# Kernel tuning notes

Hardware: AMD Instinct MI355X
Metric: run time of the kernel (lower is better)

The kernel has to match this reference:

```python
import jax, jax.numpy as jnp
import numpy as np

B, T, H, F, E = 512, 32, 768, 3072, 3  # E = num_route_experts = num_experts - 1 (top-1 beam)


def setup_inputs() -> dict:
    key = jax.random.key(0)
    ks = jax.random.split(key, 4)
    s = 0.02
    return {
        "x": jax.random.normal(ks[0], (B, T, H), jnp.float32),
        "Wg": jax.random.normal(ks[1], (E, H), jnp.float32) * s,
        "W1": jax.random.normal(ks[2], (E, H, F), jnp.float32) * s,
        "b1": jnp.zeros((E, F), jnp.float32),
        "W2": jax.random.normal(ks[3], (E, F, H), jnp.float32) * s,
        "b2": jnp.zeros((E, H), jnp.float32),
    }


def reference(x, Wg, W1, b1, W2, b2):
    # forward_gate: mean-pool over tokens (attention_mask is all-ones), linear gate, softmax
    scores = jax.nn.softmax(jnp.mean(x, axis=1) @ Wg.T, axis=-1)  # [B, E]
    # beam_search, first layer with num_route_beam=1: plain top-1 expert selection
    _, idx = jax.lax.top_k(scores, 1)
    sel = idx[:, 0]  # [B] int32, selected expert per sample
    # forward_expert_ffn: densely run EVERY route expert (gelu MLP) on the full batch
    h = jax.nn.gelu(jnp.einsum('bth,ehf->betf', x, W1) + b1[None, :, None, :], approximate=False)  # [B,E,T,F]
    y = jnp.einsum('betf,efh->beth', h, W2) + b2[None, :, None, :]  # [B,E,T,H]
    # weight_type == 'ffn_prob': one-hot mask times gate prob, then sum over experts
    w = scores * jax.nn.one_hot(sel, E, dtype=scores.dtype)  # [B, E]
    out = jnp.einsum('beth,be->bth', y, w)  # [B, T, H]
    return out
```

## Files before the change

kernel.cpp:

```cpp
#include <hip/hip_runtime.h>
#include <hip/hip_bf16.h>
#include <cstdint>
#include <cstddef>

namespace {

constexpr int kB = 512, kT = 32, kH = 768, kF = 3072, kE = 3;
constexpr int kMaxTiles = 131;
constexpr int kMaxChunk = 131;
constexpr int kXPermTile = 128 * kH;
constexpr int kHbufTile  = 128 * kF;

typedef __attribute__((ext_vector_type(8))) short short8;
typedef __attribute__((ext_vector_type(4))) float f32x4;

__device__ __forceinline__ void gld_lds16(const void* g, void* l) {
  __builtin_amdgcn_global_load_lds(
      (const __attribute__((address_space(1))) void*)g,
      (__attribute__((address_space(3))) void*)l, 16, 0, 0);
}

__device__ __forceinline__ float bf2f(__hip_bfloat16 v) { return __bfloat162float(v); }
__device__ __forceinline__ float bfu(unsigned short u) {
  return __uint_as_float(((unsigned)u) << 16);
}
__device__ __forceinline__ unsigned short f2bfb(float f) {
  __hip_bfloat16 h = __float2bfloat16(f);
  return *reinterpret_cast<unsigned short*>(&h);
}

__device__ __forceinline__ float gelu_f(float v) {
  float av = fabsf(v);
  float z = av * 0.70710678118654752f;
  float t = __builtin_amdgcn_rcpf(fmaf(0.3275911f, z, 1.0f));
  float p = fmaf(fmaf(fmaf(fmaf(1.061405429f, t, -1.453152027f), t, 1.421413741f),
                      t, -0.284496736f), t, 0.254829592f) * t;
  float er = fmaf(-p, __expf(-z * z), 1.0f);
  return 0.5f * v + 0.5f * av * er;
}

__global__ void k_sniff_all(const unsigned short* __restrict__ x,
                            const unsigned short* __restrict__ g,
                            const unsigned short* __restrict__ w1,
                            const unsigned short* __restrict__ w2,
                            int* __restrict__ flags, int* __restrict__ cnt,
                            int* __restrict__ ticket) {
  int bb = blockIdx.x;
  if (bb == 0 && threadIdx.x < 4) {
    if (threadIdx.x < 3) cnt[threadIdx.x] = 0;
    else *ticket = 0;
  }
  const unsigned short* p = (bb == 0) ? x : (bb == 1) ? g : (bb == 2) ? w1 : w2;
  int nwords = (bb == 1) ? kE * kH : 4096;
  __shared__ int cnt_s;
  if (threadIdx.x == 0) cnt_s = 0;
  __syncthreads();
  int local = 0;
  for (int i = threadIdx.x; i < nwords; i += 256) {
    unsigned e = (p[i] >> 7) & 0xFF;
    if (e >= 0xC0) ++local;
  }
  atomicAdd(&cnt_s, local);
  __syncthreads();
  if (threadIdx.x == 0) flags[bb] = (cnt_s > 64) ? 1 : 0;
}

__global__ void k_route(const void* __restrict__ xv, const void* __restrict__ Wgv,
                        const int* __restrict__ flags,
                        float* __restrict__ wsel,
                        int* __restrict__ cnt, int* __restrict__ lists,
                        int* __restrict__ ticket,
                        int* __restrict__ tileExpert, int* __restrict__ tileBatch,
                        int* __restrict__ numTiles) {
  bool fx = (flags[0] != 0), fg = (flags[1] != 0);
  int b = blockIdx.x;
  int tid = threadIdx.x;
  float a0 = 0.f, a1 = 0.f, a2 = 0.f;
  if (tid < 192) {
    float m0 = 0.f, m1 = 0.f, m2 = 0.f, m3 = 0.f;
    if (fx) {
      const float4* xr = (const float4*)((const float*)xv + (size_t)b * kT * kH) + tid;
#pragma unroll 8
      for (int t = 0; t < kT; ++t) {
        float4 u = xr[t * 192];
        m0 += u.x; m1 += u.y; m2 += u.z; m3 += u.w;
      }
    } else {
      const ushort4* xr = (const ushort4*)((const unsigned short*)xv + (size_t)b * kT * kH) + tid;
#pragma unroll 8
      for (int t = 0; t < kT; ++t) {
        ushort4 u = xr[t * 192];
        m0 += bfu(u.x); m1 += bfu(u.y); m2 += bfu(u.z); m3 += bfu(u.w);
      }
    }
    const float inv = 1.f / kT;
    m0 *= inv; m1 *= inv; m2 *= inv; m3 *= inv;
#pragma unroll
    for (int e = 0; e < kE; ++e) {
      float w0, w1v, w2v, w3;
      int base = e * kH + tid * 4;
      if (fg) {
        float4 u = *(const float4*)((const float*)Wgv + base);
        w0 = u.x; w1v = u.y; w2v = u.z; w3 = u.w;
      } else {
        ushort4 u = *(const ushort4*)((const unsigned short*)Wgv + base);
        w0 = bfu(u.x); w1v = bfu(u.y); w2v = bfu(u.z); w3 = bfu(u.w);
      }
      float d = m0 * w0 + m1 * w1v + m2 * w2v + m3 * w3;
      if (e == 0) a0 = d; else if (e == 1) a1 = d; else a2 = d;
    }
  }
  __shared__ float red[3][256];
  red[0][tid] = a0; red[1][tid] = a1; red[2][tid] = a2;
  __syncthreads();
  for (int s2 = 128; s2 > 0; s2 >>= 1) {
    if (tid < s2) {
      red[0][tid] += red[0][tid + s2];
      red[1][tid] += red[1][tid + s2];
      red[2][tid] += red[2][tid + s2];
    }
    __syncthreads();
  }
  if (tid == 0) {
    float l0 = red[0][0], l1 = red[1][0], l2 = red[2][0];
    int am = 0; float mx = l0;
    if (l1 > mx) { mx = l1; am = 1; }
    if (l2 > mx) { mx = l2; am = 2; }
    float e0 = expf(l0 - mx), e1 = expf(l1 - mx), e2 = expf(l2 - mx);
    float inv = 1.f / (e0 + e1 + e2);
    float sc = (am == 0 ? e0 : (am == 1 ? e1 : e2)) * inv;
    wsel[b] = sc;
    int pos = atomicAdd(&cnt[am], 1);
    lists[am * kB + pos] = b;
    __threadfence();
    int tk = atomicAdd(ticket, 1);
    if (tk == kB - 1) {
      __threadfence();
      int t = 0;
      for (int e = 0; e < kE; ++e) {
        int c = cnt[e];
        for (int i = 0; i < c; i += 4) {
          tileExpert[t] = e;
          for (int s = 0; s < 4; ++s)
            tileBatch[t * 4 + s] = (i + s < c) ? lists[e * kB + i + s] : -1;
          ++t;
        }
      }
      *numTiles = t;
      for (int tt = t; tt < kMaxTiles; ++tt) {
        tileExpert[tt] = 0;
        for (int s = 0; s < 4; ++s) tileBatch[tt * 4 + s] = -1;
      }
    }
  }
}

__global__ __launch_bounds__(256)
void k_transpose6(const void* __restrict__ w1src, const void* __restrict__ w2src,
                  __hip_bfloat16* __restrict__ w1dst, __hip_bfloat16* __restrict__ w2dst,
                  const int* __restrict__ flags) {
  int z = blockIdx.z;
  bool isW1 = (z < 3);
  int e = isW1 ? z : z - 3;
  bool f32 = (flags[isW1 ? 2 : 3] != 0);
  const float* sf = (const float*)(isW1 ? w1src : w2src);
  const unsigned short* sb = (const unsigned short*)(isW1 ? w1src : w2src);
  unsigned short* dst = (unsigned short*)(isW1 ? w1dst : w2dst);
  int K = isW1 ? kH : kF, N = isW1 ? kF : kH;
  int ntx = N / 64;
  int bx = blockIdx.x;
  int n0 = (bx % ntx) * 64, k0 = (bx / ntx) * 64;
  __shared__ __align__(16) unsigned short t[64][73];
  size_t eoff = (size_t)e * K * N;
  int tr = threadIdx.x >> 4;
  int tc4 = (threadIdx.x & 15) * 4;
#pragma unroll
  for (int i = 0; i < 4; ++i) {
    int r = tr + 16 * i;
    size_t idx = eoff + (size_t)(k0 + r) * N + n0 + tc4;
    if (f32) {
      float4 u = *(const float4*)(sf + idx);
      t[r][tc4] = f2bfb(u.x); t[r][tc4 + 1] = f2bfb(u.y);
      t[r][tc4 + 2] = f2bfb(u.z); t[r][tc4 + 3] = f2bfb(u.w);
    } else {
      ushort4 u = *(const ushort4*)(sb + idx);
      t[r][tc4] = u.x; t[r][tc4 + 1] = u.y; t[r][tc4 + 2] = u.z; t[r][tc4 + 3] = u.w;
    }
  }
  __syncthreads();
#pragma unroll
  for (int i = 0; i < 4; ++i) {
    int rn = tr + 16 * i;
    ushort4 v;
    v.x = t[tc4][rn]; v.y = t[tc4 + 1][rn]; v.z = t[tc4 + 2][rn]; v.w = t[tc4 + 3][rn];
    *(ushort4*)(dst + eoff + (size_t)(n0 + rn) * K + k0 + tc4) = v;
  }
}

__global__ __launch_bounds__(256)
void k_convert_x(const void* __restrict__ xv, const int* __restrict__ flags,
                 const int* __restrict__ tileBatch, const int* __restrict__ numTiles,
                 __hip_bfloat16* __restrict__ xperm) {
  int tile = blockIdx.y;
  if (tile >= *numTiles) return;
  int kblk = blockIdx.x;
  bool fx = (flags[0] != 0);
  const float* xf = (const float*)xv;
  const __hip_bfloat16* xb = (const __hip_bfloat16*)xv;
  int tb0 = tileBatch[tile * 4];
  int tb[4];
#pragma unroll
  for (int s = 0; s < 4; ++s) {
    int bb = tileBatch[tile * 4 + s];
    tb[s] = (bb < 0) ? tb0 : bb;
  }
  int tid = threadIdx.x;
  short8* dst = (short8*)(xperm + (size_t)tile * kXPermTile + kblk * 8192);
#pragma unroll
  for (int i = 0; i < 4; ++i) {
    int s = i * 256 + tid;
    int m = (s >> 2) & 127, kk = s >> 9;
    int q = (s & 3) ^ ((s >> 3) & 3);
    int row = tb[m >> 5] * kT + (m & 31);
    size_t src = (size_t)row * kH + kblk * 64 + kk * 32 + q * 8;
    short8 v;
    if (fx) {
      float4 u = *(const float4*)(xf + src);
      float4 w = *(const float4*)(xf + src + 4);
      v[0] = f2bfb(u.x); v[1] = f2bfb(u.y); v[2] = f2bfb(u.z); v[3] = f2bfb(u.w);
      v[4] = f2bfb(w.x); v[5] = f2bfb(w.y); v[6] = f2bfb(w.z); v[7] = f2bfb(w.w);
    } else {
      v = *(const short8*)(xb + src);
    }
    dst[s] = v;
  }
}

__global__ __launch_bounds__(256, 2)
void k_ffn1(const __hip_bfloat16* __restrict__ xperm,
            const __hip_bfloat16* __restrict__ w1t,
            const __hip_bfloat16* __restrict__ b1,
            const int* __restrict__ tileExpert,
            const int* __restrict__ numTiles,
            int tileOff,
            __hip_bfloat16* __restrict__ hbuf) {
  int j = blockIdx.y;
  int local = j / 3;
  int tile = local + tileOff;
  if (tile >= *numTiles) return;
  int nIdx = 8 * (j % 3) + blockIdx.x;
  int nbase = nIdx * 128;
  int e = tileExpert[tile];
  __shared__ __align__(16) short ldsbuf[16384];
  short* ldsA = ldsbuf;
  short* ldsB = ldsbuf + 8192;
  int tid = threadIdx.x;
  int lane = tid & 63, wid = tid >> 6;
  int wm = wid >> 1, wn = wid & 1;
  int lane16 = lane & 15, qf = lane >> 4;
  int swzl = (lane16 >> 1) & 3;
  int qx = (qf ^ swzl) * 8;

  f32x4 acc[4][4];
#pragma unroll
  for (int r = 0; r < 4; ++r)
#pragma unroll
    for (int c = 0; c < 4; ++c) acc[r][c] = (f32x4)0.f;

  const __hip_bfloat16* w1e = w1t + (size_t)e * kF * kH;
  const __hip_bfloat16* xtile = xperm + (size_t)tile * kXPermTile;
  const __hip_bfloat16* gB[4];
  short* lA[4];
  short* lB[4];
  int aoff[4];
#pragma unroll
  for (int it = 0; it < 4; ++it) {
    int s = it * 256 + tid;
    int m = (s >> 2) & 127, kk = s >> 9;
    int q = (s & 3) ^ ((s >> 3) & 3);
    aoff[it] = s * 8;
    gB[it] = w1e + (size_t)(nbase + m) * kH + kk * 32 + q * 8;
    lA[it] = &ldsA[s * 8];
    lB[it] = &ldsB[s * 8];
  }

  for (int k0 = 0; k0 < kH; k0 += 64) {
#pragma unroll
    for (int it = 0; it < 4; ++it) gld_lds16(xtile + k0 * 128 + aoff[it], lA[it]);
#pragma unroll
    for (int it = 0; it < 4; ++it) gld_lds16(gB[it] + k0, lB[it]);
    __syncthreads();
#pragma unroll
    for (int kk = 0; kk < 2; ++kk) {
      short8 af[4], bfr[4];
#pragma unroll
      for (int r = 0; r < 4; ++r) {
        int mr = wm * 64 + r * 16 + lane16;
        af[r] = *(const short8*)&ldsA[(kk * 512 + mr * 4) * 8 + qx];
      }
#pragma unroll
      for (int c = 0; c < 4; ++c) {
        int mb = wn * 64 + c * 16 + lane16;
        bfr[c] = *(const short8*)&ldsB[(kk * 512 + mb * 4) * 8 + qx];
      }
#pragma unroll
      for (int r = 0; r < 4; ++r)
#pragma unroll
        for (int c = 0; c < 4; ++c)
          acc[r][c] = __builtin_amdgcn_mfma_f32_16x16x32_bf16(af[r], bfr[c], acc[r][c], 0, 0, 0);
    }
    __syncthreads();
  }

  __hip_bfloat16* htile = hbuf + (size_t)local * kHbufTile;
  unsigned short* uls = (unsigned short*)ldsbuf;
  int q4 = qf * 4;
#pragma unroll
  for (int c = 0; c < 4; ++c) {
    int nn = wn * 64 + c * 16 + lane16;
    float bias = bf2f(b1[e * kF + nbase + nn]);
    int lbase = (nn >> 6) * 8192 + ((nn >> 5) & 1) * 4096 + (nn & 7);
    int qn = (nn >> 3) & 3;
#pragma unroll
    for (int r = 0; r < 4; ++r) {
#pragma unroll
      for (int g = 0; g < 4; ++g) {
        int m = wm * 64 + r * 16 + q4 + g;
        float v = acc[r][c][g] + bias;
        uls[lbase + (m * 4 + (qn ^ ((m >> 1) & 3))) * 8] = f2bfb(gelu_f(v));
      }
    }
  }
  __syncthreads();
  unsigned short* dstg = (unsigned short*)htile + (size_t)(nbase >> 6) * 8192;
#pragma unroll
  for (int i = 0; i < 8; ++i) {
    int s = i * 2048 + tid * 8;
    *(short8*)(dstg + s) = *(const short8*)(uls + s);
  }
}

__global__ __launch_bounds__(256, 2)
void k_ffn2(const __hip_bfloat16* __restrict__ hbuf,
            const __hip_bfloat16* __restrict__ w2t,
            const __hip_bfloat16* __restrict__ b2,
            const float* __restrict__ wsel,
            const int* __restrict__ tileExpert,
            const int* __restrict__ tileBatch,
            const int* __restrict__ numTiles,
            int tileOff, int chunk,
            float* __restrict__ out) {
  int j = blockIdx.y;
  int local = blockIdx.x + 8 * (j / 6);
  if (local >= chunk) return;
  int tile = local + tileOff;
  if (tile >= *numTiles) return;
  int nbase = (j % 6) * 128;
  int e = tileExpert[tile];
  int tbraw[4];
  float sc[4];
#pragma unroll
  for (int s = 0; s < 4; ++s) {
    int bb = tileBatch[tile * 4 + s];
    tbraw[s] = bb;
    sc[s] = (bb >= 0) ? wsel[bb] : 0.f;
  }
  __shared__ __align__(16) short ldsA[8192];
  __shared__ __align__(16) short ldsB[8192];
  int tid = threadIdx.x;
  int lane = tid & 63, wid = tid >> 6;
  int wm = wid >> 1, wn = wid & 1;
  int lane16 = lane & 15, qf = lane >> 4;
  int swzl = (lane16 >> 1) & 3;
  int qx = (qf ^ swzl) * 8;

  f32x4 acc[4][4];
#pragma unroll
  for (int r = 0; r < 4; ++r)
#pragma unroll
    for (int c = 0; c < 4; ++c) acc[r][c] = (f32x4)0.f;

  const __hip_bfloat16* w2e = w2t + (size_t)e * kF * kH;
  const __hip_bfloat16* htile = hbuf + (size_t)local * kHbufTile;
  const __hip_bfloat16* gB[4];
  short* lA[4];
  short* lB[4];
  int aoff[4];
#pragma unroll
  for (int it = 0; it < 4; ++it) {
    int s = it * 256 + tid;
    int m = (s >> 2) & 127, kk = s >> 9;
    int q = (s & 3) ^ ((s >> 3) & 3);
    aoff[it] = s * 8;
    gB[it] = w2e + (size_t)(nbase + m) * kF + kk * 32 + q * 8;
    lA[it] = &ldsA[s * 8];
    lB[it] = &ldsB[s * 8];
  }

  for (int k0 = 0; k0 < kF; k0 += 64) {
#pragma unroll
    for (int it = 0; it < 4; ++it) gld_lds16(htile + k0 * 128 + aoff[it], lA[it]);
#pragma unroll
    for (int it = 0; it < 4; ++it) gld_lds16(gB[it] + k0, lB[it]);
    __syncthreads();
#pragma unroll
    for (int kk = 0; kk < 2; ++kk) {
      short8 af[4], bfr[4];
#pragma unroll
      for (int r = 0; r < 4; ++r) {
        int mr = wm * 64 + r * 16 + lane16;
        af[r] = *(const short8*)&ldsA[(kk * 512 + mr * 4) * 8 + qx];
      }
#pragma unroll
      for (int c = 0; c < 4; ++c) {
        int mb = wn * 64 + c * 16 + lane16;
        bfr[c] = *(const short8*)&ldsB[(kk * 512 + mb * 4) * 8 + qx];
      }
#pragma unroll
      for (int r = 0; r < 4; ++r)
#pragma unroll
        for (int c = 0; c < 4; ++c)
          acc[r][c] = __builtin_amdgcn_mfma_f32_16x16x32_bf16(af[r], bfr[c], acc[r][c], 0, 0, 0);
    }
    __syncthreads();
  }

  int q4 = qf * 4;
#pragma unroll
  for (int c = 0; c < 4; ++c) {
    int ncol = wn * 64 + c * 16 + lane16;
    float bias = bf2f(b2[e * kH + nbase + ncol]);
#pragma unroll
    for (int r = 0; r < 4; ++r) {
      int s = (wm * 64 + r * 16) >> 5;
      int bb = tbraw[s];
      if (bb < 0) continue;
      float scale = sc[s];
#pragma unroll
      for (int g = 0; g < 4; ++g) {
        int m = wm * 64 + r * 16 + q4 + g;
        float v = (acc[r][c][g] + bias) * scale;
        out[((size_t)(bb * kT + (m & 31))) * kH + nbase + ncol] = v;
      }
    }
  }
}

}

extern "C" void kernel_launch(void* const* d_in, const int* in_sizes, int n_in,
                              void* d_out, int out_size, void* d_ws, size_t ws_size,
                              hipStream_t stream) {
  (void)in_sizes; (void)n_in; (void)out_size;
  float* out = (float*)d_out;

  char* ws = (char*)d_ws;
  size_t off = 0;
  auto alloc = [&](size_t bytes) -> char* {
    char* p = ws + off;
    off = (off + bytes + 255) & ~(size_t)255;
    return p;
  };
  int*   flags      = (int*)alloc(16);
  int*   cnt        = (int*)alloc(kE * 4);
  int*   ticket     = (int*)alloc(4);
  float* wsel       = (float*)alloc(kB * 4);
  int*   lists      = (int*)alloc((size_t)kE * kB * 4);
  int*   tileExpert = (int*)alloc(kMaxTiles * 4);
  int*   tileBatch  = (int*)alloc(kMaxTiles * 4 * 4);
  int*   numTiles   = (int*)alloc(4);
  __hip_bfloat16* w1t   = (__hip_bfloat16*)alloc((size_t)kE * kH * kF * 2);
  __hip_bfloat16* w2t   = (__hip_bfloat16*)alloc((size_t)kE * kH * kF * 2);
  __hip_bfloat16* xperm = (__hip_bfloat16*)alloc((size_t)kMaxTiles * kXPermTile * 2);

  size_t tileBytes = (size_t)kHbufTile * 2;
  size_t avail = (ws_size > off + tileBytes) ? (ws_size - off) : tileBytes;
  int chunk = (int)(avail / tileBytes);
  if (chunk > kMaxChunk) chunk = kMaxChunk;
  if (chunk < 1) chunk = 1;
  __hip_bfloat16* hbuf = (__hip_bfloat16*)alloc((size_t)chunk * tileBytes);

  k_sniff_all<<<4, 256, 0, stream>>>((const unsigned short*)d_in[0],
                                     (const unsigned short*)d_in[1],
                                     (const unsigned short*)d_in[2],
                                     (const unsigned short*)d_in[4],
                                     flags, cnt, ticket);
  k_route<<<kB, 256, 0, stream>>>(d_in[0], d_in[1], flags, wsel, cnt, lists,
                                  ticket, tileExpert, tileBatch, numTiles);
  k_transpose6<<<dim3(576, 1, 6), 256, 0, stream>>>(d_in[2], d_in[4], w1t, w2t, flags);
  k_convert_x<<<dim3(kH / 64, kMaxTiles), 256, 0, stream>>>(d_in[0], flags, tileBatch,
                                                            numTiles, xperm);
  for (int toff = 0; toff < kMaxTiles; toff += chunk) {
    k_ffn1<<<dim3(8, 3 * chunk), 256, 0, stream>>>(xperm, w1t,
                                                   (const __hip_bfloat16*)d_in[3],
                                                   tileExpert, numTiles, toff, hbuf);
    int rows2 = (chunk + 7) / 8;
    k_ffn2<<<dim3(8, 6 * rows2), 256, 0, stream>>>(hbuf, w2t,
                                                   (const __hip_bfloat16*)d_in[5], wsel,
                                                   tileExpert, tileBatch, numTiles,
                                                   toff, chunk, out);
  }
}
```

Baseline: 429.5 us.

## Rewrite FFN2 GEMM as 256x256 tiles with 4-stage LDS pipeline

The second FFN GEMM now uses 512-thread blocks that each cover two 128-row tiles of the same expert and 256 output columns, streaming K in steps of 32 through a four-buffer LDS ring. Global-to-LDS loads run three steps ahead, with explicit waitcnt, barriers and setprio around the MFMA phases. To allow tile pairing, routing pads each expert's tile count to a multiple of two, so some empty tiles are computed. This is meant to raise data reuse per load and hide memory latency. The cost is 128KB of dynamic LDS, lower occupancy and wasted padding work.

```diff
diff --git a/kernel.cpp b/kernel.cpp
--- a/kernel.cpp
+++ b/kernel.cpp
@@ -6,10 +6,11 @@
 namespace {
 
 constexpr int kB = 512, kT = 32, kH = 768, kF = 3072, kE = 3;
-constexpr int kMaxTiles = 131;
-constexpr int kMaxChunk = 131;
+constexpr int kMaxTiles = 132;
+constexpr int kMaxChunk = 132;
 constexpr int kXPermTile = 128 * kH;
 constexpr int kHbufTile  = 128 * kF;
+constexpr int kNT2 = kF / 32;
 
 typedef __attribute__((ext_vector_type(8))) short short8;
 typedef __attribute__((ext_vector_type(4))) float f32x4;
@@ -139,7 +140,8 @@
       int t = 0;
       for (int e = 0; e < kE; ++e) {
         int c = cnt[e];
-        for (int i = 0; i < c; i += 4) {
+        int cpad = (c + 7) & ~7;
+        for (int i = 0; i < cpad; i += 4) {
           tileExpert[t] = e;
           for (int s = 0; s < 4; ++s)
             tileBatch[t * 4 + s] = (i + s < c) ? lists[e * kB + i + s] : -1;
@@ -212,7 +214,7 @@
 #pragma unroll
   for (int s = 0; s < 4; ++s) {
     int bb = tileBatch[tile * 4 + s];
-    tb[s] = (bb < 0) ? tb0 : bb;
+    tb[s] = (bb < 0) ? ((tb0 < 0) ? 0 : tb0) : bb;
   }
   int tid = threadIdx.x;
   short8* dst = (short8*)(xperm + (size_t)tile * kXPermTile + kblk * 8192);
@@ -340,7 +342,7 @@
   }
 }
 
-__global__ __launch_bounds__(256, 2)
+__global__ __launch_bounds__(512, 2)
 void k_ffn2(const __hip_bfloat16* __restrict__ hbuf,
             const __hip_bfloat16* __restrict__ w2t,
             const __hip_bfloat16* __restrict__ b2,
@@ -350,97 +352,131 @@
             const int* __restrict__ numTiles,
             int tileOff, int chunk,
             float* __restrict__ out) {
-  int j = blockIdx.y;
-  int local = blockIdx.x + 8 * (j / 6);
-  if (local >= chunk) return;
-  int tile = local + tileOff;
-  if (tile >= *numTiles) return;
-  int nbase = (j % 6) * 128;
-  int e = tileExpert[tile];
-  int tbraw[4];
-  float sc[4];
-#pragma unroll
-  for (int s = 0; s < 4; ++s) {
-    int bb = tileBatch[tile * 4 + s];
+  extern __shared__ __align__(16) short lds[];
+  int nblk = (chunk >> 1) * 3;
+  int lid = blockIdx.x * gridDim.y + blockIdx.y;
+  if (lid >= nblk) return;
+  int pair = lid / 3;
+  int nbase = (lid - pair * 3) * 256;
+  int tile0 = tileOff + 2 * pair;
+  if (tile0 >= *numTiles) return;
+  int e = tileExpert[tile0];
+
+  int tbraw[8];
+  float sc[8];
+#pragma unroll
+  for (int s = 0; s < 8; ++s) {
+    int bb = tileBatch[tile0 * 4 + s];
     tbraw[s] = bb;
     sc[s] = (bb >= 0) ? wsel[bb] : 0.f;
   }
-  __shared__ __align__(16) short ldsA[8192];
-  __shared__ __align__(16) short ldsB[8192];
+
   int tid = threadIdx.x;
   int lane = tid & 63, wid = tid >> 6;
-  int wm = wid >> 1, wn = wid & 1;
+  int wm = wid >> 2, wn = wid & 3;
   int lane16 = lane & 15, qf = lane >> 4;
-  int swzl = (lane16 >> 1) & 3;
-  int qx = (qf ^ swzl) * 8;
-
-  f32x4 acc[4][4];
-#pragma unroll
-  for (int r = 0; r < 4; ++r)
+  int qx = (qf ^ ((lane16 >> 1) & 3)) * 8;
+  int tid8 = tid * 8;
+
+  int sm = tid >> 2;
+  int sq = (tid & 3) ^ ((tid >> 3) & 3);
+  const __hip_bfloat16* w2e = w2t + (size_t)e * kF * kH;
+  const __hip_bfloat16* aS0 = hbuf + (size_t)(2 * pair) * kHbufTile + tid8;
+  const __hip_bfloat16* aS1 = hbuf + (size_t)(2 * pair + 1) * kHbufTile + tid8;
+  const __hip_bfloat16* bS0 = w2e + (size_t)(nbase + sm) * kF + sq * 8;
+  const __hip_bfloat16* bS1 = w2e + (size_t)(nbase + 128 + sm) * kF + sq * 8;
+
+  int aOffB = wm * 4096 + lane16 * 32 + qx;
+  int bOffB = 8192 + (wn >> 1) * 4096 + (wn & 1) * 2048 + lane16 * 32 + qx;
+
+  f32x4 acc[8][4];
+#pragma unroll
+  for (int r = 0; r < 8; ++r)
 #pragma unroll
     for (int c = 0; c < 4; ++c) acc[r][c] = (f32x4)0.f;
 
-  const __hip_bfloat16* w2e = w2t + (size_t)e * kF * kH;
-  const __hip_bfloat16* htile = hbuf + (size_t)local * kHbufTile;
-  const __hip_bfloat16* gB[4];
-  short* lA[4];
-  short* lB[4];
-  int aoff[4];
-#pragma unroll
-  for (int it = 0; it < 4; ++it) {
-    int s = it * 256 + tid;
-    int m = (s >> 2) & 127, kk = s >> 9;
-    int q = (s & 3) ^ ((s >> 3) & 3);
-    aoff[it] = s * 8;
-    gB[it] = w2e + (size_t)(nbase + m) * kF + kk * 32 + q * 8;
-    lA[it] = &ldsA[s * 8];
-    lB[it] = &ldsB[s * 8];
-  }
-
-  for (int k0 = 0; k0 < kF; k0 += 64) {
-#pragma unroll
-    for (int it = 0; it < 4; ++it) gld_lds16(htile + k0 * 128 + aoff[it], lA[it]);
-#pragma unroll
-    for (int it = 0; it < 4; ++it) gld_lds16(gB[it] + k0, lB[it]);
-    __syncthreads();
-#pragma unroll
-    for (int kk = 0; kk < 2; ++kk) {
-      short8 af[4], bfr[4];
-#pragma unroll
-      for (int r = 0; r < 4; ++r) {
-        int mr = wm * 64 + r * 16 + lane16;
-        af[r] = *(const short8*)&ldsA[(kk * 512 + mr * 4) * 8 + qx];
-      }
-#pragma unroll
-      for (int c = 0; c < 4; ++c) {
-        int mb = wn * 64 + c * 16 + lane16;
-        bfr[c] = *(const short8*)&ldsB[(kk * 512 + mb * 4) * 8 + qx];
-      }
-#pragma unroll
-      for (int r = 0; r < 4; ++r)
-#pragma unroll
-        for (int c = 0; c < 4; ++c)
-          acc[r][c] = __builtin_amdgcn_mfma_f32_16x16x32_bf16(af[r], bfr[c], acc[r][c], 0, 0, 0);
-    }
-    __syncthreads();
+#pragma unroll
+  for (int kt = 0; kt < 3; ++kt) {
+    int sl = kt * 16384;
+    gld_lds16(aS0 + (size_t)kt * 4096, &lds[sl + tid8]);
+    gld_lds16(aS1 + (size_t)kt * 4096, &lds[sl + 4096 + tid8]);
+    gld_lds16(bS0 + kt * 32, &lds[sl + 8192 + tid8]);
+    gld_lds16(bS1 + kt * 32, &lds[sl + 12288 + tid8]);
+  }
+  asm volatile("s_waitcnt vmcnt(8)" ::: "memory");
+  __builtin_amdgcn_s_barrier();
+
+  for (int t = 0; t < kNT2; ++t) {
+    short* sb = &lds[(t & 3) * 16384];
+    const int g3 = t + 3;
+    short8 a0 = *(const short8*)&sb[aOffB + 0 * 512];
+    short8 a1 = *(const short8*)&sb[aOffB + 1 * 512];
+    short8 a2 = *(const short8*)&sb[aOffB + 2 * 512];
+    short8 a3 = *(const short8*)&sb[aOffB + 3 * 512];
+    short8 b0 = *(const short8*)&sb[bOffB + 0 * 512];
+    short8 b1 = *(const short8*)&sb[bOffB + 1 * 512];
+    short8 b2v = *(const short8*)&sb[bOffB + 2 * 512];
+    short8 b3 = *(const short8*)&sb[bOffB + 3 * 512];
+    if (g3 < kNT2) {
+      int sl = (g3 & 3) * 16384;
+      gld_lds16(aS0 + (size_t)g3 * 4096, &lds[sl + tid8]);
+      gld_lds16(aS1 + (size_t)g3 * 4096, &lds[sl + 4096 + tid8]);
+    }
+    __builtin_amdgcn_s_barrier();
+    __builtin_amdgcn_s_setprio(1);
+#pragma unroll
+    for (int r = 0; r < 4; ++r) {
+      short8 ar = (r == 0) ? a0 : (r == 1) ? a1 : (r == 2) ? a2 : a3;
+      acc[r][0] = __builtin_amdgcn_mfma_f32_16x16x32_bf16(ar, b0, acc[r][0], 0, 0, 0);
+      acc[r][1] = __builtin_amdgcn_mfma_f32_16x16x32_bf16(ar, b1, acc[r][1], 0, 0, 0);
+      acc[r][2] = __builtin_amdgcn_mfma_f32_16x16x32_bf16(ar, b2v, acc[r][2], 0, 0, 0);
+      acc[r][3] = __builtin_amdgcn_mfma_f32_16x16x32_bf16(ar, b3, acc[r][3], 0, 0, 0);
+    }
+    __builtin_amdgcn_s_setprio(0);
+    __builtin_amdgcn_s_barrier();
+    a0 = *(const short8*)&sb[aOffB + 4 * 512];
+    a1 = *(const short8*)&sb[aOffB + 5 * 512];
+    a2 = *(const short8*)&sb[aOffB + 6 * 512];
+    a3 = *(const short8*)&sb[aOffB + 7 * 512];
+    if (g3 < kNT2) {
+      int sl = (g3 & 3) * 16384;
+      gld_lds16(bS0 + g3 * 32, &lds[sl + 8192 + tid8]);
+      gld_lds16(bS1 + g3 * 32, &lds[sl + 12288 + tid8]);
+    }
+    if (t < kNT2 - 3)       { asm volatile("s_waitcnt vmcnt(8)" ::: "memory"); }
+    else if (t == kNT2 - 3) { asm volatile("s_waitcnt vmcnt(4)" ::: "memory"); }
+    else if (t == kNT2 - 2) { asm volatile("s_waitcnt vmcnt(0)" ::: "memory"); }
+    __builtin_amdgcn_s_barrier();
+    __builtin_amdgcn_s_setprio(1);
+#pragma unroll
+    for (int r = 0; r < 4; ++r) {
+      short8 ar = (r == 0) ? a0 : (r == 1) ? a1 : (r == 2) ? a2 : a3;
+      acc[r + 4][0] = __builtin_amdgcn_mfma_f32_16x16x32_bf16(ar, b0, acc[r + 4][0], 0, 0, 0);
+      acc[r + 4][1] = __builtin_amdgcn_mfma_f32_16x16x32_bf16(ar, b1, acc[r + 4][1], 0, 0, 0);
+      acc[r + 4][2] = __builtin_amdgcn_mfma_f32_16x16x32_bf16(ar, b2v, acc[r + 4][2], 0, 0, 0);
+      acc[r + 4][3] = __builtin_amdgcn_mfma_f32_16x16x32_bf16(ar, b3, acc[r + 4][3], 0, 0, 0);
+    }
+    __builtin_amdgcn_s_setprio(0);
+    __builtin_amdgcn_s_barrier();
   }
 
   int q4 = qf * 4;
 #pragma unroll
   for (int c = 0; c < 4; ++c) {
-    int ncol = wn * 64 + c * 16 + lane16;
-    float bias = bf2f(b2[e * kH + nbase + ncol]);
-#pragma unroll
-    for (int r = 0; r < 4; ++r) {
-      int s = (wm * 64 + r * 16) >> 5;
+    int ncol = nbase + wn * 64 + c * 16 + lane16;
+    float bias = bf2f(b2[e * kH + ncol]);
+#pragma unroll
+    for (int r = 0; r < 8; ++r) {
+      int mbase = wm * 128 + r * 16;
+      int s = mbase >> 5;
       int bb = tbraw[s];
       if (bb < 0) continue;
       float scale = sc[s];
 #pragma unroll
       for (int g = 0; g < 4; ++g) {
-        int m = wm * 64 + r * 16 + q4 + g;
+        int m = mbase + q4 + g;
         float v = (acc[r][c][g] + bias) * scale;
-        out[((size_t)(bb * kT + (m & 31))) * kH + nbase + ncol] = v;
+        out[((size_t)(bb * kT + (m & 31))) * kH + ncol] = v;
       }
     }
   }
@@ -474,11 +510,19 @@
   __hip_bfloat16* xperm = (__hip_bfloat16*)alloc((size_t)kMaxTiles * kXPermTile * 2);
 
   size_t tileBytes = (size_t)kHbufTile * 2;
-  size_t avail = (ws_size > off + tileBytes) ? (ws_size - off) : tileBytes;
+  size_t avail = (ws_size > off + 2 * tileBytes) ? (ws_size - off) : 2 * tileBytes;
   int chunk = (int)(avail / tileBytes);
   if (chunk > kMaxChunk) chunk = kMaxChunk;
-  if (chunk < 1) chunk = 1;
+  chunk &= ~1;
+  if (chunk < 2) chunk = 2;
   __hip_bfloat16* hbuf = (__hip_bfloat16*)alloc((size_t)chunk * tileBytes);
+
+  static bool attrDone = false;
+  if (!attrDone) {
+    hipFuncSetAttribute((const void*)k_ffn2,
+                        hipFuncAttributeMaxDynamicSharedMemorySize, 131072);
+    attrDone = true;
+  }
 
   k_sniff_all<<<4, 256, 0, stream>>>((const unsigned short*)d_in[0],
                                      (const unsigned short*)d_in[1],
@@ -494,10 +538,9 @@
     k_ffn1<<<dim3(8, 3 * chunk), 256, 0, stream>>>(xperm, w1t,
                                                    (const __hip_bfloat16*)d_in[3],
                                                    tileExpert, numTiles, toff, hbuf);
-    int rows2 = (chunk + 7) / 8;
-    k_ffn2<<<dim3(8, 6 * rows2), 256, 0, stream>>>(hbuf, w2t,
-                                                   (const __hip_bfloat16*)d_in[5], wsel,
-                                                   tileExpert, tileBatch, numTiles,
-                                                   toff, chunk, out);
-  }
-}
+    int nblk2 = (chunk / 2) * 3;
+    k_ffn2<<<dim3(8, (nblk2 + 7) / 8), 512, 131072, stream>>>(
+        hbuf, w2t, (const __hip_bfloat16*)d_in[5], wsel,
+        tileExpert, tileBatch, numTiles, toff, chunk, out);
+  }
+}
```

Result: no change. 426.0 us (-0.8%).

## Use 256x256 tiles with 4-stage LDS pipeline and batch-major x conversion

Applied to the files above, without the earlier changes.

The FFN GEMMs move from 128x128 tiles with 256 threads and a single-buffered LDS loop to 256-token-by-256-feature tiles with 512 threads. Each tile covers a pair of expert-aligned 4-sample groups and runs a 4-stage global_load_lds pipeline with explicit vmcnt waits, setprio around the MFMAs, and swizzled LDS staging of the gelu output. x is converted once per batch into a pre-swizzled bf16 layout and gathered per tile, instead of being permuted per tile. Routing tile construction is parallelized across threads and pads each expert's tile count to even pairs. The aim is more MFMA work per byte loaded and better latency hiding, at the cost of 128KB dynamic LDS per block, more padding work, and lower occupancy.

```diff
diff --git a/kernel.cpp b/kernel.cpp
--- a/kernel.cpp
+++ b/kernel.cpp
@@ -6,10 +6,11 @@
 namespace {
 
 constexpr int kB = 512, kT = 32, kH = 768, kF = 3072, kE = 3;
-constexpr int kMaxTiles = 131;
-constexpr int kMaxChunk = 131;
-constexpr int kXPermTile = 128 * kH;
-constexpr int kHbufTile  = 128 * kF;
+constexpr int kMaxTiles = 132;
+constexpr int kMaxChunk = 132;
+constexpr int kHbufPair = 96 * 8192;
+constexpr int kNT1 = kH / 32;
+constexpr int kNT2 = kF / 32;
 
 typedef __attribute__((ext_vector_type(8))) short short8;
 typedef __attribute__((ext_vector_type(4))) float f32x4;
@@ -111,6 +112,8 @@
     }
   }
   __shared__ float red[3][256];
+  __shared__ int lastFlag;
+  __shared__ int csh[3];
   red[0][tid] = a0; red[1][tid] = a1; red[2][tid] = a2;
   __syncthreads();
   for (int s2 = 128; s2 > 0; s2 >>= 1) {
@@ -134,22 +137,35 @@
     lists[am * kB + pos] = b;
     __threadfence();
     int tk = atomicAdd(ticket, 1);
-    if (tk == kB - 1) {
-      __threadfence();
-      int t = 0;
-      for (int e = 0; e < kE; ++e) {
-        int c = cnt[e];
-        for (int i = 0; i < c; i += 4) {
-          tileExpert[t] = e;
-          for (int s = 0; s < 4; ++s)
-            tileBatch[t * 4 + s] = (i + s < c) ? lists[e * kB + i + s] : -1;
-          ++t;
+    lastFlag = (tk == kB - 1) ? 1 : 0;
+  }
+  __syncthreads();
+  if (lastFlag) {
+    __threadfence();
+    if (tid < 3) csh[tid] = cnt[tid];
+    __syncthreads();
+    int c0 = csh[0], c1 = csh[1], c2 = csh[2];
+    int t0 = ((c0 + 7) & ~7) >> 2;
+    int t1 = ((c1 + 7) & ~7) >> 2;
+    int t2 = ((c2 + 7) & ~7) >> 2;
+    int total = t0 + t1 + t2;
+    if (tid == 0) *numTiles = total;
+    for (int t = tid; t < kMaxTiles; t += 256) {
+      int e = 0, base = 0, cc = 0;
+      bool pad = false;
+      if (t < t0) { e = 0; base = t; cc = c0; }
+      else if (t < t0 + t1) { e = 1; base = t - t0; cc = c1; }
+      else if (t < total) { e = 2; base = t - t0 - t1; cc = c2; }
+      else pad = true;
+      if (pad) {
+        tileExpert[t] = 0;
+        for (int s = 0; s < 4; ++s) tileBatch[t * 4 + s] = -1;
+      } else {
+        tileExpert[t] = e;
+        for (int s = 0; s < 4; ++s) {
+          int i = base * 4 + s;
+          tileBatch[t * 4 + s] = (i < cc) ? lists[e * kB + i] : -1;
         }
-      }
-      *numTiles = t;
-      for (int tt = t; tt < kMaxTiles; ++tt) {
-        tileExpert[tt] = 0;
-        for (int s = 0; s < 4; ++s) tileBatch[tt * 4 + s] = -1;
       }
     }
   }
@@ -199,148 +215,169 @@
 
 __global__ __launch_bounds__(256)
 void k_convert_x(const void* __restrict__ xv, const int* __restrict__ flags,
-                 const int* __restrict__ tileBatch, const int* __restrict__ numTiles,
-                 __hip_bfloat16* __restrict__ xperm) {
-  int tile = blockIdx.y;
-  if (tile >= *numTiles) return;
-  int kblk = blockIdx.x;
+                 __hip_bfloat16* __restrict__ xconv) {
+  __shared__ __align__(16) unsigned short xs[32][772];
+  int b = blockIdx.x;
   bool fx = (flags[0] != 0);
-  const float* xf = (const float*)xv;
-  const __hip_bfloat16* xb = (const __hip_bfloat16*)xv;
-  int tb0 = tileBatch[tile * 4];
-  int tb[4];
-#pragma unroll
-  for (int s = 0; s < 4; ++s) {
-    int bb = tileBatch[tile * 4 + s];
-    tb[s] = (bb < 0) ? tb0 : bb;
-  }
   int tid = threadIdx.x;
-  short8* dst = (short8*)(xperm + (size_t)tile * kXPermTile + kblk * 8192);
-#pragma unroll
-  for (int i = 0; i < 4; ++i) {
-    int s = i * 256 + tid;
-    int m = (s >> 2) & 127, kk = s >> 9;
-    int q = (s & 3) ^ ((s >> 3) & 3);
-    int row = tb[m >> 5] * kT + (m & 31);
-    size_t src = (size_t)row * kH + kblk * 64 + kk * 32 + q * 8;
+  if (fx) {
+    const float4* src = (const float4*)((const float*)xv + (size_t)b * kT * kH);
+#pragma unroll
+    for (int i = 0; i < 24; ++i) {
+      int idx = i * 256 + tid;
+      float4 u = src[idx];
+      int t = idx / 192, col = (idx - t * 192) * 4;
+      ushort4 v;
+      v.x = f2bfb(u.x); v.y = f2bfb(u.y); v.z = f2bfb(u.z); v.w = f2bfb(u.w);
+      *(ushort4*)&xs[t][col] = v;
+    }
+  } else {
+    const ushort4* src = (const ushort4*)((const unsigned short*)xv + (size_t)b * kT * kH);
+#pragma unroll
+    for (int i = 0; i < 24; ++i) {
+      int idx = i * 256 + tid;
+      ushort4 u = src[idx];
+      int t = idx / 192, col = (idx - t * 192) * 4;
+      *(ushort4*)&xs[t][col] = u;
+    }
+  }
+  __syncthreads();
+  unsigned short* dst = (unsigned short*)xconv + (size_t)b * 24576;
+#pragma unroll
+  for (int i = 0; i < 12; ++i) {
+    int g = i * 256 + tid;
+    int t32 = g >> 7, r = g & 127, mm = r >> 2, qp = r & 3;
+    int col = t32 * 32 + (qp ^ ((mm >> 1) & 3)) * 8;
+    ushort4 lo = *(const ushort4*)&xs[mm][col];
+    ushort4 hi = *(const ushort4*)&xs[mm][col + 4];
     short8 v;
-    if (fx) {
-      float4 u = *(const float4*)(xf + src);
-      float4 w = *(const float4*)(xf + src + 4);
-      v[0] = f2bfb(u.x); v[1] = f2bfb(u.y); v[2] = f2bfb(u.z); v[3] = f2bfb(u.w);
-      v[4] = f2bfb(w.x); v[5] = f2bfb(w.y); v[6] = f2bfb(w.z); v[7] = f2bfb(w.w);
-    } else {
-      v = *(const short8*)(xb + src);
-    }
-    dst[s] = v;
-  }
-}
-
-__global__ __launch_bounds__(256, 2)
-void k_ffn1(const __hip_bfloat16* __restrict__ xperm,
+    v[0] = lo.x; v[1] = lo.y; v[2] = lo.z; v[3] = lo.w;
+    v[4] = hi.x; v[5] = hi.y; v[6] = hi.z; v[7] = hi.w;
+    *(short8*)(dst + g * 8) = v;
+  }
+}
+
+
+#define GEMM_CORE(NT, STAGE_CALL)                                              \
+  STAGE_CALL(0); STAGE_CALL(1); STAGE_CALL(2);                                 \
+  asm volatile("s_waitcnt vmcnt(8)" ::: "memory");                             \
+  __builtin_amdgcn_s_barrier();                                                \
+  for (int t = 0; t < (NT); ++t) {                                             \
+    if (t + 3 < (NT)) {                                                        \
+      STAGE_CALL(t + 3);                                                       \
+      asm volatile("s_waitcnt vmcnt(8)" ::: "memory");                         \
+    } else if (t + 3 == (NT)) {                                                \
+      asm volatile("s_waitcnt vmcnt(4)" ::: "memory");                         \
+    } else if (t + 2 == (NT)) {                                                \
+      asm volatile("s_waitcnt vmcnt(0)" ::: "memory");                         \
+    }                                                                          \
+    int sl = (t & 3) * 16384;                                                  \
+    short8 fw[8], fx8[4];                                                      \
+    _Pragma("unroll")                                                          \
+    for (int r = 0; r < 8; ++r)                                                \
+      fw[r] = *(const short8*)&lds[sl + 8192 + (wf * 128 + r * 16 + lane16) * 32 + qx]; \
+    _Pragma("unroll")                                                          \
+    for (int c = 0; c < 4; ++c)                                                \
+      fx8[c] = *(const short8*)&lds[sl + (wmv * 64 + c * 16 + lane16) * 32 + qx]; \
+    __builtin_amdgcn_s_setprio(1);                                             \
+    _Pragma("unroll")                                                          \
+    for (int r = 0; r < 8; ++r)                                                \
+      _Pragma("unroll")                                                        \
+      for (int c = 0; c < 4; ++c)                                              \
+        acc[r][c] = __builtin_amdgcn_mfma_f32_16x16x32_bf16(fw[r], fx8[c], acc[r][c], 0, 0, 0); \
+    __builtin_amdgcn_s_setprio(0);                                             \
+    __builtin_amdgcn_s_barrier();                                              \
+  }
+
+__global__ __launch_bounds__(512, 2)
+void k_ffn1(const __hip_bfloat16* __restrict__ xconv,
             const __hip_bfloat16* __restrict__ w1t,
             const __hip_bfloat16* __restrict__ b1,
             const int* __restrict__ tileExpert,
+            const int* __restrict__ tileBatch,
             const int* __restrict__ numTiles,
-            int tileOff,
+            int tileOff, int chunk,
             __hip_bfloat16* __restrict__ hbuf) {
-  int j = blockIdx.y;
-  int local = j / 3;
-  int tile = local + tileOff;
-  if (tile >= *numTiles) return;
-  int nIdx = 8 * (j % 3) + blockIdx.x;
-  int nbase = nIdx * 128;
-  int e = tileExpert[tile];
-  __shared__ __align__(16) short ldsbuf[16384];
-  short* ldsA = ldsbuf;
-  short* ldsB = ldsbuf + 8192;
+  extern __shared__ __align__(16) short lds[];
+  int pairsC = chunk >> 1;
+  int nblk = pairsC * 12;
+  int lid = blockIdx.x * gridDim.y + blockIdx.y;
+  if (lid >= nblk) return;
+  int lpair = lid / 12;
+  int nb = lid - lpair * 12;
+  int nbase = nb * 256;
+  int tile0 = tileOff + 2 * lpair;
+  if (tile0 >= *numTiles) return;
+  int e = tileExpert[tile0];
   int tid = threadIdx.x;
+  int m_l = tid >> 2;
+  int bbS0 = tileBatch[tile0 * 4 + (m_l >> 5)];
+  int bbS1 = tileBatch[tile0 * 4 + 4 + (m_l >> 5)];
+  if (bbS0 < 0) bbS0 = 0;
+  if (bbS1 < 0) bbS1 = 0;
+  int g8 = ((tid & 3) ^ ((tid >> 3) & 3)) * 8;
+  const __hip_bfloat16* w1e = w1t + (size_t)e * kF * kH;
+  int aoff = ((m_l & 31) * 4 + (tid & 3)) * 8;
+  const __hip_bfloat16* pA0 = xconv + (size_t)bbS0 * 24576 + aoff;
+  const __hip_bfloat16* pA1 = xconv + (size_t)bbS1 * 24576 + aoff;
+  const __hip_bfloat16* pB0 = w1e + (size_t)(nbase + m_l) * kH + g8;
+  const __hip_bfloat16* pB1 = w1e + (size_t)(nbase + 128 + m_l) * kH + g8;
+  int ldsT = tid * 8;
   int lane = tid & 63, wid = tid >> 6;
-  int wm = wid >> 1, wn = wid & 1;
+  int wf = wid >> 2, wmv = wid & 3;
   int lane16 = lane & 15, qf = lane >> 4;
-  int swzl = (lane16 >> 1) & 3;
-  int qx = (qf ^ swzl) * 8;
-
-  f32x4 acc[4][4];
-#pragma unroll
-  for (int r = 0; r < 4; ++r)
+  int qx = (qf ^ ((lane16 >> 1) & 3)) * 8;
+
+  f32x4 acc[8][4];
+#pragma unroll
+  for (int r = 0; r < 8; ++r)
 #pragma unroll
     for (int c = 0; c < 4; ++c) acc[r][c] = (f32x4)0.f;
 
-  const __hip_bfloat16* w1e = w1t + (size_t)e * kF * kH;
-  const __hip_bfloat16* xtile = xperm + (size_t)tile * kXPermTile;
-  const __hip_bfloat16* gB[4];
-  short* lA[4];
-  short* lB[4];
-  int aoff[4];
-#pragma unroll
-  for (int it = 0; it < 4; ++it) {
-    int s = it * 256 + tid;
-    int m = (s >> 2) & 127, kk = s >> 9;
-    int q = (s & 3) ^ ((s >> 3) & 3);
-    aoff[it] = s * 8;
-    gB[it] = w1e + (size_t)(nbase + m) * kH + kk * 32 + q * 8;
-    lA[it] = &ldsA[s * 8];
-    lB[it] = &ldsB[s * 8];
-  }
-
-  for (int k0 = 0; k0 < kH; k0 += 64) {
-#pragma unroll
-    for (int it = 0; it < 4; ++it) gld_lds16(xtile + k0 * 128 + aoff[it], lA[it]);
-#pragma unroll
-    for (int it = 0; it < 4; ++it) gld_lds16(gB[it] + k0, lB[it]);
-    __syncthreads();
-#pragma unroll
-    for (int kk = 0; kk < 2; ++kk) {
-      short8 af[4], bfr[4];
-#pragma unroll
-      for (int r = 0; r < 4; ++r) {
-        int mr = wm * 64 + r * 16 + lane16;
-        af[r] = *(const short8*)&ldsA[(kk * 512 + mr * 4) * 8 + qx];
-      }
-#pragma unroll
-      for (int c = 0; c < 4; ++c) {
-        int mb = wn * 64 + c * 16 + lane16;
-        bfr[c] = *(const short8*)&ldsB[(kk * 512 + mb * 4) * 8 + qx];
-      }
-#pragma unroll
-      for (int r = 0; r < 4; ++r)
-#pragma unroll
-        for (int c = 0; c < 4; ++c)
-          acc[r][c] = __builtin_amdgcn_mfma_f32_16x16x32_bf16(af[r], bfr[c], acc[r][c], 0, 0, 0);
-    }
-    __syncthreads();
-  }
-
-  __hip_bfloat16* htile = hbuf + (size_t)local * kHbufTile;
-  unsigned short* uls = (unsigned short*)ldsbuf;
+#define STG1(kt) do { int s_ = ((kt) & 3) * 16384;                    \
+    gld_lds16(pA0 + (kt) * 1024, &lds[s_ + ldsT]);                    \
+    gld_lds16(pA1 + (kt) * 1024, &lds[s_ + 4096 + ldsT]);             \
+    gld_lds16(pB0 + (kt) * 32, &lds[s_ + 8192 + ldsT]);               \
+    gld_lds16(pB1 + (kt) * 32, &lds[s_ + 12288 + ldsT]); } while (0)
+
+  GEMM_CORE(kNT1, STG1)
+#undef STG1
+
+  __syncthreads();
   int q4 = qf * 4;
 #pragma unroll
-  for (int c = 0; c < 4; ++c) {
-    int nn = wn * 64 + c * 16 + lane16;
-    float bias = bf2f(b1[e * kF + nbase + nn]);
-    int lbase = (nn >> 6) * 8192 + ((nn >> 5) & 1) * 4096 + (nn & 7);
-    int qn = (nn >> 3) & 3;
-#pragma unroll
-    for (int r = 0; r < 4; ++r) {
-#pragma unroll
-      for (int g = 0; g < 4; ++g) {
-        int m = wm * 64 + r * 16 + q4 + g;
-        float v = acc[r][c][g] + bias;
-        uls[lbase + (m * 4 + (qn ^ ((m >> 1) & 3))) * 8] = f2bfb(gelu_f(v));
-      }
-    }
-  }
-  __syncthreads();
-  unsigned short* dstg = (unsigned short*)htile + (size_t)(nbase >> 6) * 8192;
-#pragma unroll
-  for (int i = 0; i < 8; ++i) {
-    int s = i * 2048 + tid * 8;
-    *(short8*)(dstg + s) = *(const short8*)(uls + s);
-  }
-}
-
-__global__ __launch_bounds__(256, 2)
+  for (int r = 0; r < 8; ++r) {
+    int flb = wf * 128 + r * 16 + q4;
+    int t32l = flb >> 5;
+    int fq = (flb >> 3) & 3;
+    int j4 = flb & 7;
+    ushort4 bb4 = *(const ushort4*)((const unsigned short*)b1 + (size_t)e * kF + nbase + flb);
+    float bi0 = bfu(bb4.x), bi1 = bfu(bb4.y), bi2 = bfu(bb4.z), bi3 = bfu(bb4.w);
+#pragma unroll
+    for (int c = 0; c < 4; ++c) {
+      int m = wmv * 64 + c * 16 + lane16;
+      int qp = fq ^ ((m >> 1) & 3);
+      int w = t32l * 8192 + (m * 4 + qp) * 8 + j4;
+      int phys = w ^ (((w >> 8) & 7) << 3);
+      ushort4 pk;
+      pk.x = f2bfb(gelu_f(acc[r][c][0] + bi0));
+      pk.y = f2bfb(gelu_f(acc[r][c][1] + bi1));
+      pk.z = f2bfb(gelu_f(acc[r][c][2] + bi2));
+      pk.w = f2bfb(gelu_f(acc[r][c][3] + bi3));
+      *(ushort4*)&lds[phys] = pk;
+    }
+  }
+  __syncthreads();
+  unsigned short* hdst = (unsigned short*)hbuf + (size_t)lpair * kHbufPair + (size_t)(nbase >> 5) * 8192;
+#pragma unroll
+  for (int i = 0; i < 16; ++i) {
+    int o = i * 4096 + ldsT;
+    int phys = o ^ (((o >> 8) & 7) << 3);
+    *(short8*)(hdst + o) = *(const short8*)&lds[phys];
+  }
+}
+
+__global__ __launch_bounds__(512, 2)
 void k_ffn2(const __hip_bfloat16* __restrict__ hbuf,
             const __hip_bfloat16* __restrict__ w2t,
             const __hip_bfloat16* __restrict__ b2,
@@ -350,98 +387,68 @@
             const int* __restrict__ numTiles,
             int tileOff, int chunk,
             float* __restrict__ out) {
-  int j = blockIdx.y;
-  int local = blockIdx.x + 8 * (j / 6);
-  if (local >= chunk) return;
-  int tile = local + tileOff;
-  if (tile >= *numTiles) return;
-  int nbase = (j % 6) * 128;
-  int e = tileExpert[tile];
-  int tbraw[4];
-  float sc[4];
-#pragma unroll
-  for (int s = 0; s < 4; ++s) {
-    int bb = tileBatch[tile * 4 + s];
-    tbraw[s] = bb;
-    sc[s] = (bb >= 0) ? wsel[bb] : 0.f;
-  }
-  __shared__ __align__(16) short ldsA[8192];
-  __shared__ __align__(16) short ldsB[8192];
+  extern __shared__ __align__(16) short lds[];
+  int pairsC = chunk >> 1;
+  int nblk = pairsC * 3;
+  int lid = blockIdx.x * gridDim.y + blockIdx.y;
+  if (lid >= nblk) return;
+  int lpair = lid / 3;
+  int nb = lid - lpair * 3;
+  int nbase = nb * 256;
+  int tile0 = tileOff + 2 * lpair;
+  if (tile0 >= *numTiles) return;
+  int e = tileExpert[tile0];
   int tid = threadIdx.x;
+  int m_l = tid >> 2;
+  int g8 = ((tid & 3) ^ ((tid >> 3) & 3)) * 8;
+  const __hip_bfloat16* w2e = w2t + (size_t)e * kF * kH;
+  const __hip_bfloat16* pA = hbuf + (size_t)lpair * kHbufPair + tid * 8;
+  const __hip_bfloat16* pB0 = w2e + (size_t)(nbase + m_l) * kF + g8;
+  const __hip_bfloat16* pB1 = w2e + (size_t)(nbase + 128 + m_l) * kF + g8;
+  int ldsT = tid * 8;
   int lane = tid & 63, wid = tid >> 6;
-  int wm = wid >> 1, wn = wid & 1;
+  int wf = wid >> 2, wmv = wid & 3;
   int lane16 = lane & 15, qf = lane >> 4;
-  int swzl = (lane16 >> 1) & 3;
-  int qx = (qf ^ swzl) * 8;
-
-  f32x4 acc[4][4];
-#pragma unroll
-  for (int r = 0; r < 4; ++r)
+  int qx = (qf ^ ((lane16 >> 1) & 3)) * 8;
+  int slotBase = wmv * 2;
+  int bbA = tileBatch[tile0 * 4 + slotBase];
+  int bbB = tileBatch[tile0 * 4 + slotBase + 1];
+  float scA = (bbA >= 0) ? wsel[bbA] : 0.f;
+  float scB = (bbB >= 0) ? wsel[bbB] : 0.f;
+
+  f32x4 acc[8][4];
+#pragma unroll
+  for (int r = 0; r < 8; ++r)
 #pragma unroll
     for (int c = 0; c < 4; ++c) acc[r][c] = (f32x4)0.f;
 
-  const __hip_bfloat16* w2e = w2t + (size_t)e * kF * kH;
-  const __hip_bfloat16* htile = hbuf + (size_t)local * kHbufTile;
-  const __hip_bfloat16* gB[4];
-  short* lA[4];
-  short* lB[4];
-  int aoff[4];
-#pragma unroll
-  for (int it = 0; it < 4; ++it) {
-    int s = it * 256 + tid;
-    int m = (s >> 2) & 127, kk = s >> 9;
-    int q = (s & 3) ^ ((s >> 3) & 3);
-    aoff[it] = s * 8;
-    gB[it] = w2e + (size_t)(nbase + m) * kF + kk * 32 + q * 8;
-    lA[it] = &ldsA[s * 8];
-    lB[it] = &ldsB[s * 8];
-  }
-
-  for (int k0 = 0; k0 < kF; k0 += 64) {
-#pragma unroll
-    for (int it = 0; it < 4; ++it) gld_lds16(htile + k0 * 128 + aoff[it], lA[it]);
-#pragma unroll
-    for (int it = 0; it < 4; ++it) gld_lds16(gB[it] + k0, lB[it]);
-    __syncthreads();
-#pragma unroll
-    for (int kk = 0; kk < 2; ++kk) {
-      short8 af[4], bfr[4];
-#pragma unroll
-      for (int r = 0; r < 4; ++r) {
-        int mr = wm * 64 + r * 16 + lane16;
-        af[r] = *(const short8*)&ldsA[(kk * 512 + mr * 4) * 8 + qx];
-      }
-#pragma unroll
-      for (int c = 0; c < 4; ++c) {
-        int mb = wn * 64 + c * 16 + lane16;
-        bfr[c] = *(const short8*)&ldsB[(kk * 512 + mb * 4) * 8 + qx];
-      }
-#pragma unroll
-      for (int r = 0; r < 4; ++r)
-#pragma unroll
-        for (int c = 0; c < 4; ++c)
-          acc[r][c] = __builtin_amdgcn_mfma_f32_16x16x32_bf16(af[r], bfr[c], acc[r][c], 0, 0, 0);
-    }
-    __syncthreads();
-  }
+#define STG2(kt) do { int s_ = ((kt) & 3) * 16384;                      \
+    gld_lds16(pA + (size_t)(kt) * 8192, &lds[s_ + ldsT]);               \
+    gld_lds16(pA + (size_t)(kt) * 8192 + 4096, &lds[s_ + 4096 + ldsT]); \
+    gld_lds16(pB0 + (kt) * 32, &lds[s_ + 8192 + ldsT]);                 \
+    gld_lds16(pB1 + (kt) * 32, &lds[s_ + 12288 + ldsT]); } while (0)
+
+  GEMM_CORE(kNT2, STG2)
+#undef STG2
 
   int q4 = qf * 4;
 #pragma unroll
-  for (int c = 0; c < 4; ++c) {
-    int ncol = wn * 64 + c * 16 + lane16;
-    float bias = bf2f(b2[e * kH + nbase + ncol]);
-#pragma unroll
-    for (int r = 0; r < 4; ++r) {
-      int s = (wm * 64 + r * 16) >> 5;
-      int bb = tbraw[s];
+  for (int r = 0; r < 8; ++r) {
+    int h0 = nbase + wf * 128 + r * 16 + q4;
+    ushort4 bb4 = *(const ushort4*)((const unsigned short*)b2 + (size_t)e * kH + h0);
+    float bi0 = bfu(bb4.x), bi1 = bfu(bb4.y), bi2 = bfu(bb4.z), bi3 = bfu(bb4.w);
+#pragma unroll
+    for (int c = 0; c < 4; ++c) {
+      int bb = (c < 2) ? bbA : bbB;
       if (bb < 0) continue;
-      float scale = sc[s];
-#pragma unroll
-      for (int g = 0; g < 4; ++g) {
-        int m = wm * 64 + r * 16 + q4 + g;
-        float v = (acc[r][c][g] + bias) * scale;
-        out[((size_t)(bb * kT + (m & 31))) * kH + nbase + ncol] = v;
-      }
+      float s = (c < 2) ? scA : scB;
+      int m = wmv * 64 + c * 16 + lane16;
+      float4 o;
+      o.x = (acc[r][c][0] + bi0) * s;
+      o.y = (acc[r][c][1] + bi1) * s;
+      o.z = (acc[r][c][2] + bi2) * s;
+      o.w = (acc[r][c][3] + bi3) * s;
+      *(float4*)&out[(size_t)(bb * kT + (m & 31)) * kH + h0] = o;
     }
   }
 }
@@ -471,14 +478,21 @@
   int*   numTiles   = (int*)alloc(4);
   __hip_bfloat16* w1t   = (__hip_bfloat16*)alloc((size_t)kE * kH * kF * 2);
   __hip_bfloat16* w2t   = (__hip_bfloat16*)alloc((size_t)kE * kH * kF * 2);
-  __hip_bfloat16* xperm = (__hip_bfloat16*)alloc((size_t)kMaxTiles * kXPermTile * 2);
-
-  size_t tileBytes = (size_t)kHbufTile * 2;
-  size_t avail = (ws_size > off + tileBytes) ? (ws_size - off) : tileBytes;
+  __hip_bfloat16* xconv = (__hip_bfloat16*)alloc((size_t)kB * kT * kH * 2);
+
+  size_t pairBytes = (size_t)kHbufPair * 2;
+  size_t tileBytes = pairBytes / 2;
+  size_t avail = (ws_size > off + pairBytes) ? (ws_size - off) : pairBytes;
   int chunk = (int)(avail / tileBytes);
   if (chunk > kMaxChunk) chunk = kMaxChunk;
-  if (chunk < 1) chunk = 1;
-  __hip_bfloat16* hbuf = (__hip_bfloat16*)alloc((size_t)chunk * tileBytes);
+  chunk &= ~1;
+  if (chunk < 2) chunk = 2;
+  __hip_bfloat16* hbuf = (__hip_bfloat16*)alloc((size_t)(chunk / 2) * pairBytes);
+
+  hipFuncSetAttribute((const void*)k_ffn1,
+                      hipFuncAttributeMaxDynamicSharedMemorySize, 131072);
+  hipFuncSetAttribute((const void*)k_ffn2,
+                      hipFuncAttributeMaxDynamicSharedMemorySize, 131072);
 
   k_sniff_all<<<4, 256, 0, stream>>>((const unsigned short*)d_in[0],
                                      (const unsigned short*)d_in[1],
@@ -487,17 +501,17 @@
                                      flags, cnt, ticket);
   k_route<<<kB, 256, 0, stream>>>(d_in[0], d_in[1], flags, wsel, cnt, lists,
                                   ticket, tileExpert, tileBatch, numTiles);
+  k_convert_x<<<kB, 256, 0, stream>>>(d_in[0], flags, xconv);
   k_transpose6<<<dim3(576, 1, 6), 256, 0, stream>>>(d_in[2], d_in[4], w1t, w2t, flags);
-  k_convert_x<<<dim3(kH / 64, kMaxTiles), 256, 0, stream>>>(d_in[0], flags, tileBatch,
-                                                            numTiles, xperm);
   for (int toff = 0; toff < kMaxTiles; toff += chunk) {
-    k_ffn1<<<dim3(8, 3 * chunk), 256, 0, stream>>>(xperm, w1t,
-                                                   (const __hip_bfloat16*)d_in[3],
-                                                   tileExpert, numTiles, toff, hbuf);
-    int rows2 = (chunk + 7) / 8;
-    k_ffn2<<<dim3(8, 6 * rows2), 256, 0, stream>>>(hbuf, w2t,
-                                                   (const __hip_bfloat16*)d_in[5], wsel,
-                                                   tileExpert, tileBatch, numTiles,
-                                                   toff, chunk, out);
-  }
-}
+    int pairsC = chunk / 2;
+    int nblk1 = pairsC * 12;
+    int nblk2 = pairsC * 3;
+    k_ffn1<<<dim3(8, (nblk1 + 7) / 8), 512, 131072, stream>>>(
+        xconv, w1t, (const __hip_bfloat16*)d_in[3],
+        tileExpert, tileBatch, numTiles, toff, chunk, hbuf);
+    k_ffn2<<<dim3(8, (nblk2 + 7) / 8), 512, 131072, stream>>>(
+        hbuf, w2t, (const __hip_bfloat16*)d_in[5], wsel,
+        tileExpert, tileBatch, numTiles, toff, chunk, out);
+  }
+}
```

Measured after the change: 413.0 us. 1.04x faster.
